# Optimization experiments

Measured on AMD Instinct MI355X. Metric: run time of the kernel, lower is better.

The kernel has to match this reference:

```python
import jax, jax.numpy as jnp
import numpy as np

ROPE_BASE = 10000.0


def _rope_cos_sin(n, d, dtype):
    # standard llama-style rotary embedding over head dim d
    inv_freq = 1.0 / (ROPE_BASE ** (jnp.arange(0, d, 2, dtype=jnp.float32) / d))
    t = jnp.arange(n, dtype=jnp.float32)
    freqs = jnp.einsum('n,f->nf', t, inv_freq)          # [N, d/2]
    emb = jnp.concatenate([freqs, freqs], axis=-1)      # [N, d]
    return jnp.cos(emb).astype(dtype), jnp.sin(emb).astype(dtype)


def _rotate_half(x):
    x1, x2 = jnp.split(x, 2, axis=-1)
    return jnp.concatenate([-x2, x1], axis=-1)


def _apply_rope(x, cos, sin):
    # x: [B, H, N, D]; cos/sin: [N, D] broadcast over B, H
    return x * cos + _rotate_half(x) * sin


def setup_inputs() -> dict:
    key = jax.random.key(0)
    k1, k2, k3 = jax.random.split(key, 3)
    B, N, dim = 2, 2048, 1024
    heads, dim_head = 16, 64
    inner = heads * dim_head
    x = jax.random.normal(k1, (B, N, dim), dtype=jnp.float32)
    w_qkv = jax.random.normal(k2, (dim, 3 * inner), dtype=jnp.float32) * (dim ** -0.5)
    w_out = jax.random.normal(k3, (inner, dim), dtype=jnp.float32) * (inner ** -0.5)
    return {"x": x, "w_qkv": w_qkv, "w_out": w_out}


def reference(x, w_qkv, w_out):
    B, N, _ = x.shape
    heads, dim_head = 16, 64
    qkv = jnp.einsum('bnd,de->bne', x, w_qkv)
    q, k, v = jnp.split(qkv, 3, axis=-1)
    def to_heads(t):
        return t.reshape(B, N, heads, dim_head).transpose(0, 2, 1, 3)  # [B,H,N,D]
    q, k, v = to_heads(q), to_heads(k), to_heads(v)
    cos, sin = _rope_cos_sin(N, dim_head, x.dtype)
    q = _apply_rope(q, cos, sin)
    k = _apply_rope(k, cos, sin)
    scale = dim_head ** -0.5
    scores = jnp.einsum('bhqd,bhkd->bhqk', q, k) * scale   # [B,H,N,N], non-causal
    attn = jax.nn.softmax(scores, axis=-1)
    out = jnp.einsum('bhqk,bhkd->bhqd', attn, v)
    out = out.transpose(0, 2, 1, 3).reshape(B, N, heads * dim_head)
    return jnp.einsum('bne,ed->bnd', out, w_out)
```

## Files before the change

### kernel.cpp

```cpp
#include <hip/hip_runtime.h>

typedef __attribute__((ext_vector_type(8))) short bf16x8;
typedef __attribute__((ext_vector_type(4))) float f32x4;

#define MFMA(a, b, c) __builtin_amdgcn_mfma_f32_16x16x32_bf16(a, b, c, 0, 0, 0)

__device__ __forceinline__ unsigned short f2bf(float f) {
    unsigned u = __builtin_bit_cast(unsigned, f);
    u += 0x7fffu + ((u >> 16) & 1u);
    return (unsigned short)(u >> 16);
}

__device__ __forceinline__ void gload16(const unsigned short* g, unsigned short* l) {
    __builtin_amdgcn_global_load_lds(
        (const __attribute__((address_space(1))) void*)g,
        (__attribute__((address_space(3))) void*)l, 16, 0, 0);
}

__device__ __forceinline__ unsigned pack_bf16(float lo, float hi) {
    unsigned a = __builtin_bit_cast(unsigned, lo) + 0x8000u;
    unsigned b = __builtin_bit_cast(unsigned, hi) + 0x8000u;
    return __builtin_amdgcn_perm(b, a, 0x07060302);
}


__global__ __launch_bounds__(256) void cvt_bf16(const float* __restrict__ in,
                                                unsigned short* __restrict__ out, int n) {
    int i = (blockIdx.x * 256 + threadIdx.x) * 4;
    if (i < n) {
        float4 f = *(const float4*)(in + i);
        ushort4 u;
        u.x = f2bf(f.x); u.y = f2bf(f.y); u.z = f2bf(f.z); u.w = f2bf(f.w);
        *(ushort4*)(out + i) = u;
    }
}

__global__ __launch_bounds__(256) void transpose_cvt(const float* __restrict__ in,
                                                     unsigned short* __restrict__ out,
                                                     int R, int C) {
    __shared__ float tile[32][33];
    const int c0 = blockIdx.x * 32, r0 = blockIdx.y * 32;
    const int tr = threadIdx.x >> 3;
    const int j4 = (threadIdx.x & 7) * 4;
    float4 f = *(const float4*)(in + (size_t)(r0 + tr) * C + c0 + j4);
    tile[tr][j4 + 0] = f.x; tile[tr][j4 + 1] = f.y;
    tile[tr][j4 + 2] = f.z; tile[tr][j4 + 3] = f.w;
    __syncthreads();
    ushort4 u;
    u.x = f2bf(tile[j4 + 0][tr]); u.y = f2bf(tile[j4 + 1][tr]);
    u.z = f2bf(tile[j4 + 2][tr]); u.w = f2bf(tile[j4 + 3][tr]);
    *(ushort4*)(out + (size_t)(c0 + tr) * R + r0 + j4) = u;
}

__global__ __launch_bounds__(256) void rope_tab(float* __restrict__ cosT,
                                                float* __restrict__ sinT) {
    int i = blockIdx.x * 256 + threadIdx.x;
    int n = i >> 5, f = i & 31;
    float ang = (float)n * exp2f((float)f * -0.4152410118609203f);
    float s, c;
    sincosf(ang, &s, &c);
    cosT[i] = c; sinT[i] = s;
}


template <int EPI>
__global__ __launch_bounds__(256, 3) void gemm_bt(const unsigned short* __restrict__ A,
                                                  const unsigned short* __restrict__ Bt,
                                                  int K, int Ncols,
                                                  unsigned short* __restrict__ oq,
                                                  unsigned short* __restrict__ ok,
                                                  unsigned short* __restrict__ ovt,
                                                  float* __restrict__ of,
                                                  const float* __restrict__ cosT,
                                                  const float* __restrict__ sinT) {
    __shared__ unsigned short As[2][128 * 32];
    __shared__ unsigned short Bs[2][128 * 32];
    const int tid = threadIdx.x;
    const int w = tid >> 6, lane = tid & 63, quad = lane >> 4, cc = lane & 15;
    const int wm = w >> 1, wn = w & 1;
    const int m0 = blockIdx.y * 128, n0 = blockIdx.x * 128;

    size_t aoff[2], boff[2];
#pragma unroll
    for (int t = 0; t < 2; t++) {
        int S = w * 128 + t * 64 + lane;
        int row = S >> 2;
        int c = (S & 3) ^ ((row >> 1) & 3);
        aoff[t] = (size_t)(m0 + row) * K + c * 8;
        boff[t] = (size_t)(n0 + row) * K + c * 8;
    }

#pragma unroll
    for (int t = 0; t < 2; t++) {
        gload16(A + aoff[t], &As[0][(w * 2 + t) * 512]);
        gload16(Bt + boff[t], &Bs[0][(w * 2 + t) * 512]);
    }
    __syncthreads();

    f32x4 acc[4][4] = {};
    const int rpos = (quad ^ ((cc >> 1) & 3)) * 8;
    const int nkt = K >> 5;

    for (int kt = 0; kt < nkt; kt++) {
        const int pb = kt & 1;
        if (kt < nkt - 1) {
            const int ko = (kt + 1) * 32;
#pragma unroll
            for (int t = 0; t < 2; t++) {
                gload16(A + aoff[t] + ko, &As[pb ^ 1][(w * 2 + t) * 512]);
                gload16(Bt + boff[t] + ko, &Bs[pb ^ 1][(w * 2 + t) * 512]);
            }
        }
        bf16x8 af[4], bf[4];
#pragma unroll
        for (int i = 0; i < 4; i++)
            af[i] = *(const bf16x8*)&As[pb][(wm * 64 + i * 16 + cc) * 32 + rpos];
#pragma unroll
        for (int i = 0; i < 4; i++)
            bf[i] = *(const bf16x8*)&Bs[pb][(wn * 64 + i * 16 + cc) * 32 + rpos];
#pragma unroll
        for (int i = 0; i < 4; i++)
#pragma unroll
            for (int j = 0; j < 4; j++)
                acc[i][j] = MFMA(af[i], bf[j], acc[i][j]);
        __syncthreads();
    }

    if (EPI == 0) {
        const int e0 = n0 + wn * 64;
        const int which = e0 >> 10;
        const int h = (e0 >> 6) & 15;
        if (which < 2) {
            unsigned short* dst = (which == 0) ? oq : ok;
            const float postscale = (which == 0) ? 0.125f : 1.0f;
#pragma unroll
            for (int mf = 0; mf < 4; mf++) {
#pragma unroll
                for (int r = 0; r < 4; r++) {
                    int mg = m0 + wm * 64 + mf * 16 + quad * 4 + r;
                    int nseq = mg & 2047, b = mg >> 11;
                    float vals[4];
#pragma unroll
                    for (int nf = 0; nf < 4; nf++) vals[nf] = acc[mf][nf][r];
                    size_t rowbase = ((size_t)(b * 16 + h) * 2048 + nseq) * 64;
#pragma unroll
                    for (int nf = 0; nf < 4; nf++) {
                        int d = nf * 16 + cc;
                        int f = d & 31;
                        float cs = cosT[nseq * 32 + f];
                        float sn = sinT[nseq * 32 + f];
                        float partner = vals[nf ^ 2];
                        float outv = (vals[nf] * cs +
                                      ((nf < 2) ? -partner : partner) * sn) * postscale;
                        dst[rowbase + d] = f2bf(outv);
                    }
                }
            }
        } else {
#pragma unroll
            for (int mf = 0; mf < 4; mf++) {
                int mg0 = m0 + wm * 64 + mf * 16 + quad * 4;
                int b = mg0 >> 11, nseq = mg0 & 2047;
#pragma unroll
                for (int nf = 0; nf < 4; nf++) {
                    int d = nf * 16 + cc;
                    ushort4 pk;
                    pk.x = f2bf(acc[mf][nf][0]);
                    pk.y = f2bf(acc[mf][nf][1]);
                    pk.z = f2bf(acc[mf][nf][2]);
                    pk.w = f2bf(acc[mf][nf][3]);
                    *(ushort4*)(ovt + ((size_t)(b * 16 + h) * 64 + d) * 2048 + nseq) = pk;
                }
            }
        }
    } else {
#pragma unroll
        for (int mf = 0; mf < 4; mf++)
#pragma unroll
            for (int nf = 0; nf < 4; nf++)
#pragma unroll
                for (int r = 0; r < 4; r++) {
                    int mg = m0 + wm * 64 + mf * 16 + quad * 4 + r;
                    of[(size_t)mg * Ncols + n0 + wn * 64 + nf * 16 + cc] = acc[mf][nf][r];
                }
    }
}


__global__ __launch_bounds__(512, 4) void attn(const unsigned short* __restrict__ q,
                                               const unsigned short* __restrict__ k,
                                               const unsigned short* __restrict__ vt,
                                               unsigned short* __restrict__ o) {
    __shared__ unsigned short ks[2][64 * 64];
    __shared__ unsigned short vs[2][64 * 64];
    __shared__ unsigned short ps[128 * 72];
    __shared__ float rsb[128];
    const int tid = threadIdx.x;
    const int w = tid >> 6, lane = tid & 63, quad = lane >> 4, cc = lane & 15;
    const int bh = blockIdx.x & 31, qt = blockIdx.x >> 5;

    const unsigned short* qg = q + ((size_t)bh * 2048 + qt * 128 + w * 16) * 64;
    bf16x8 aq[2];
#pragma unroll
    for (int kc = 0; kc < 2; kc++)
        aq[kc] = *(const bf16x8*)(qg + cc * 64 + kc * 32 + quad * 8);

    const int S = w * 64 + lane;
    const int row = S >> 3;
    const int c = (S & 7) ^ (row & 7);
    const int koff = row * 64 + c * 8;
    const int voff = row * 2048 + c * 8;

    const unsigned short* kg0 = k + (size_t)bh * 2048 * 64;
    const unsigned short* vg0 = vt + (size_t)bh * 64 * 2048;

    gload16(kg0 + koff, &ks[0][w * 512]);
    __syncthreads();

    f32x4 oacc[4] = {};
    float rs = 0.f;
    bf16x8 apP[2];

    auto qk = [&](const unsigned short* kbuf, f32x4 s2[4]) {
#pragma unroll
        for (int kc = 0; kc < 2; kc++)
#pragma unroll
            for (int nf = 0; nf < 4; nf++) {
                bf16x8 bk = *(const bf16x8*)&kbuf[(nf * 16 + cc) * 64 +
                                                  ((kc * 4 + quad) ^ (cc & 7)) * 8];
                s2[nf] = MFMA(bk, aq[kc], s2[nf]);
            }
    };
    auto pv = [&](const unsigned short* vbuf, const bf16x8 ap[2]) {
#pragma unroll
        for (int kc = 0; kc < 2; kc++)
#pragma unroll
            for (int df = 0; df < 4; df++) {
                bf16x8 bv = *(const bf16x8*)&vbuf[(df * 16 + cc) * 64 +
                                                  ((kc * 4 + quad) ^ (cc & 7)) * 8];
                oacc[df] = MFMA(ap[kc], bv, oacc[df]);
            }
    };
    auto softmax_pack = [&](const f32x4 s2[4], bf16x8 apC[2]) {
        unsigned X[4][2];
#pragma unroll
        for (int nf = 0; nf < 4; nf++) {
            float p0 = __builtin_amdgcn_exp2f(
                __builtin_fmaf(s2[nf][0], 1.44269504f, -11.54156036f));
            float p1 = __builtin_amdgcn_exp2f(
                __builtin_fmaf(s2[nf][1], 1.44269504f, -11.54156036f));
            float p2 = __builtin_amdgcn_exp2f(
                __builtin_fmaf(s2[nf][2], 1.44269504f, -11.54156036f));
            float p3 = __builtin_amdgcn_exp2f(
                __builtin_fmaf(s2[nf][3], 1.44269504f, -11.54156036f));
            rs += (p0 + p1) + (p2 + p3);
            X[nf][0] = pack_bf16(p0, p1);
            X[nf][1] = pack_bf16(p2, p3);
        }
#pragma unroll
        for (int kc = 0; kc < 2; kc++) {
            unsigned a0 = X[kc * 2][0], b0 = X[kc * 2 + 1][0];
            unsigned a1 = X[kc * 2][1], b1 = X[kc * 2 + 1][1];
            asm("v_permlane32_swap_b32 %0, %1" : "+v"(a0), "+v"(b0));
            asm("v_permlane16_swap_b32 %0, %1" : "+v"(a0), "+v"(b0));
            asm("v_permlane32_swap_b32 %0, %1" : "+v"(a1), "+v"(b1));
            asm("v_permlane16_swap_b32 %0, %1" : "+v"(a1), "+v"(b1));
            uint4 dd;
            dd.x = a0; dd.y = a1; dd.z = b0; dd.w = b1;
            apC[kc] = __builtin_bit_cast(bf16x8, dd);
        }
    };

    gload16(kg0 + 4096 + koff, &ks[1][w * 512]);
    gload16(vg0 + voff, &vs[0][w * 512]);
    {
        f32x4 s2[4] = {};
        __builtin_amdgcn_s_setprio(1);
        qk(ks[0], s2);
        __builtin_amdgcn_s_setprio(0);
        softmax_pack(s2, apP);
    }
    __syncthreads();

    for (int kt = 1; kt < 32; kt++) {
        if (kt < 31)
            gload16(kg0 + (kt + 1) * 4096 + koff, &ks[(kt + 1) & 1][w * 512]);
        gload16(vg0 + kt * 64 + voff, &vs[kt & 1][w * 512]);

        f32x4 s2[4] = {};
        __builtin_amdgcn_s_setprio(1);
        qk(ks[kt & 1], s2);
        pv(vs[(kt - 1) & 1], apP);
        __builtin_amdgcn_s_setprio(0);

        bf16x8 apC[2];
        softmax_pack(s2, apC);
        apP[0] = apC[0];
        apP[1] = apC[1];
        __syncthreads();
    }

    __builtin_amdgcn_s_setprio(1);
    pv(vs[1], apP);
    __builtin_amdgcn_s_setprio(0);

    rs += __shfl_xor(rs, 16, 64);
    rs += __shfl_xor(rs, 32, 64);
    if (quad == 0) rsb[w * 16 + cc] = rs;

    {
        f32x4 rv = *(const f32x4*)&rsb[w * 16 + quad * 4];
        f32x4 inv;
#pragma unroll
        for (int r = 0; r < 4; r++) inv[r] = 1.0f / rv[r];
#pragma unroll
        for (int r = 0; r < 4; r++)
#pragma unroll
            for (int df = 0; df < 4; df++)
                ps[(w * 16 + quad * 4 + r) * 72 + df * 16 + cc] =
                    f2bf(oacc[df][r] * inv[r]);
    }
    __syncthreads();
    {
        const int b = bh >> 4, h = bh & 15;
        int row2 = tid >> 2, seg = tid & 3;
        unsigned short* og =
            o + ((size_t)(b * 2048 + qt * 128 + row2)) * 1024 + h * 64 + seg * 16;
#pragma unroll
        for (int j = 0; j < 2; j++)
            *(uint4*)(og + j * 8) = *(const uint4*)&ps[row2 * 72 + seg * 16 + j * 8];
    }
}


extern "C" void kernel_launch(void* const* d_in, const int* in_sizes, int n_in,
                              void* d_out, int out_size, void* d_ws, size_t ws_size,
                              hipStream_t stream) {
    const float* x = (const float*)d_in[0];
    const float* w_qkv = (const float*)d_in[1];
    const float* w_out = (const float*)d_in[2];
    float* out = (float*)d_out;

    unsigned short* xb    = (unsigned short*)d_ws;
    unsigned short* wqkvT = xb + 4096 * 1024;
    unsigned short* woutT = wqkvT + 3072 * 1024;
    unsigned short* qb    = woutT + 1024 * 1024;
    unsigned short* kb    = qb + 2 * 16 * 2048 * 64;
    unsigned short* vtb   = kb + 2 * 16 * 2048 * 64;
    unsigned short* ob    = vtb + 2 * 16 * 2048 * 64;
    float* cosT = (float*)(ob + 4096 * 1024);
    float* sinT = cosT + 2048 * 32;

    rope_tab<<<256, 256, 0, stream>>>(cosT, sinT);
    cvt_bf16<<<4096, 256, 0, stream>>>(x, xb, 4096 * 1024);
    transpose_cvt<<<dim3(96, 32), 256, 0, stream>>>(w_qkv, wqkvT, 1024, 3072);
    transpose_cvt<<<dim3(32, 32), 256, 0, stream>>>(w_out, woutT, 1024, 1024);
    gemm_bt<0><<<dim3(24, 32), 256, 0, stream>>>(xb, wqkvT, 1024, 3072,
                                                 qb, kb, vtb, nullptr, cosT, sinT);
    attn<<<512, 512, 0, stream>>>(qb, kb, vtb, ob);
    gemm_bt<1><<<dim3(8, 32), 256, 0, stream>>>(ob, woutT, 1024, 1024,
                                                nullptr, nullptr, nullptr, out,
                                                nullptr, nullptr);
}
```

Baseline: 188.1 us.

## Triple-buffer K/V tiles with explicit vmcnt waits in attention loop

Switches the attention K and V shared-memory staging from double to triple buffering. Loads are issued two tiles ahead and waited on with explicit s_waitcnt vmcnt plus a raw s_barrier instead of __syncthreads. The software-pipelined QK/PV skew across iterations is removed, so each iteration now computes QK, softmax and PV on the same tile. This trades extra LDS (reducing possible occupancy), and the loss of cross-iteration MFMA/softmax overlap, for deeper memory prefetch. It also relies on vmcnt counting only these loads, so the hand-written waits must match the number of loads in flight.

```diff
diff --git a/kernel.cpp b/kernel.cpp
--- a/kernel.cpp
+++ b/kernel.cpp
@@ -191,8 +191,8 @@
                                                const unsigned short* __restrict__ k,
                                                const unsigned short* __restrict__ vt,
                                                unsigned short* __restrict__ o) {
-    __shared__ unsigned short ks[2][64 * 64];
-    __shared__ unsigned short vs[2][64 * 64];
+    __shared__ unsigned short ks[3][64 * 64];
+    __shared__ unsigned short vs[3][64 * 64];
     __shared__ unsigned short ps[128 * 72];
     __shared__ float rsb[128];
     const int tid = threadIdx.x;
@@ -215,11 +215,12 @@
     const unsigned short* vg0 = vt + (size_t)bh * 64 * 2048;
 
     gload16(kg0 + koff, &ks[0][w * 512]);
-    __syncthreads();
+    gload16(vg0 + voff, &vs[0][w * 512]);
+    gload16(kg0 + 4096 + koff, &ks[1][w * 512]);
+    gload16(vg0 + 64 + voff, &vs[1][w * 512]);
 
     f32x4 oacc[4] = {};
     float rs = 0.f;
-    bf16x8 apP[2];
 
     auto qk = [&](const unsigned short* kbuf, f32x4 s2[4]) {
 #pragma unroll
@@ -271,38 +272,36 @@
         }
     };
 
-    gload16(kg0 + 4096 + koff, &ks[1][w * 512]);
-    gload16(vg0 + voff, &vs[0][w * 512]);
-    {
+    int cur = 0;
+    int wrt = 2;
+    for (int kt = 0; kt < 32; kt++) {
+        if (kt < 31) {
+            asm volatile("s_waitcnt vmcnt(2)" ::: "memory");
+        } else {
+            asm volatile("s_waitcnt vmcnt(0)" ::: "memory");
+        }
+        __builtin_amdgcn_s_barrier();
+
+        if (kt <= 29) {
+            gload16(kg0 + (kt + 2) * 4096 + koff, &ks[wrt][w * 512]);
+            gload16(vg0 + (kt + 2) * 64 + voff, &vs[wrt][w * 512]);
+        }
+
         f32x4 s2[4] = {};
         __builtin_amdgcn_s_setprio(1);
-        qk(ks[0], s2);
+        qk(&ks[cur][0], s2);
         __builtin_amdgcn_s_setprio(0);
-        softmax_pack(s2, apP);
-    }
-    __syncthreads();
-
-    for (int kt = 1; kt < 32; kt++) {
-        if (kt < 31)
-            gload16(kg0 + (kt + 1) * 4096 + koff, &ks[(kt + 1) & 1][w * 512]);
-        gload16(vg0 + kt * 64 + voff, &vs[kt & 1][w * 512]);
-
-        f32x4 s2[4] = {};
+
+        bf16x8 ap[2];
+        softmax_pack(s2, ap);
+
         __builtin_amdgcn_s_setprio(1);
-        qk(ks[kt & 1], s2);
-        pv(vs[(kt - 1) & 1], apP);
+        pv(&vs[cur][0], ap);
         __builtin_amdgcn_s_setprio(0);
 
-        bf16x8 apC[2];
-        softmax_pack(s2, apC);
-        apP[0] = apC[0];
-        apP[1] = apC[1];
-        __syncthreads();
-    }
-
-    __builtin_amdgcn_s_setprio(1);
-    pv(vs[1], apP);
-    __builtin_amdgcn_s_setprio(0);
+        cur = (cur == 2) ? 0 : cur + 1;
+        wrt = (wrt == 2) ? 0 : wrt + 1;
+    }
 
     rs += __shfl_xor(rs, 16, 64);
     rs += __shfl_xor(rs, 32, 64);
```

Result: no change. 188.9 us (+0.4%).
